# Kernel optimization log

Hardware: AMD Instinct MI355X
Metric: run time of the kernel (lower is better)

The kernel has to match this reference:

```python
import jax, jax.numpy as jnp
import numpy as np
import math

IN_C, OUT_C, K, STYLE_DIM = 512, 512, 3, 512
EPS = 1e-8
SCALE = 1.0 / math.sqrt(IN_C * K * K)


def setup_inputs() -> dict:
    key = jax.random.key(0)
    k1, k2, k3, k4, k5 = jax.random.split(key, 5)
    x = jax.random.normal(k1, (8, IN_C, 64, 64), dtype=jnp.float32)
    style = jax.random.normal(k2, (8, STYLE_DIM), dtype=jnp.float32)
    weight = jax.random.normal(k3, (1, OUT_C, IN_C, K, K), dtype=jnp.float32)
    # nn.Linear(style_dim, in_channels): weight [in_channels, style_dim], bias [in_channels]
    lim = 1.0 / math.sqrt(STYLE_DIM)
    style_w = jax.random.uniform(k4, (IN_C, STYLE_DIM), dtype=jnp.float32, minval=-lim, maxval=lim)
    style_b = jax.random.uniform(k5, (IN_C,), dtype=jnp.float32, minval=-lim, maxval=lim)
    return {"x": x, "style": style, "weight": weight, "style_w": style_w, "style_b": style_b}


def _conv_one(xi, wi):
    # xi: [C,H,W], wi: [O,I,K,K]
    out = jax.lax.conv_general_dilated(
        xi[None], wi, window_strides=(1, 1), padding="SAME",
        dimension_numbers=("NCHW", "OIHW", "NCHW"))
    return out[0]


def reference(x, style, weight, style_w, style_b):
    N = x.shape[0]
    s = style @ style_w.T + style_b                      # [N, C_in]
    w = weight * SCALE                                    # [1,O,I,K,K]
    w = w * s[:, None, :, None, None]                     # [N,O,I,K,K]
    demod = jax.lax.rsqrt(jnp.sum(w * w, axis=(2, 3, 4)) + EPS)  # [N,O]
    w = w * demod[:, :, None, None, None]
    out = jax.vmap(_conv_one)(x, w)                       # [N,O,H,W]
    return out
```

## Files before the change

kernel.cpp:

```cpp
#include <hip/hip_runtime.h>
#include <stdint.h>

typedef unsigned short u16;
typedef __bf16 bf16x8 __attribute__((ext_vector_type(8)));
typedef float f32x4 __attribute__((ext_vector_type(4)));

#define SCALE_F 0.014731391274719742f

#define S_OFF   0u
#define WM_OFF  1081344u
#define XS_OFF  38830080u
#define WS_NEED 74514432u

__device__ __forceinline__ u16 f2bf(float f) {
  union { float f; uint32_t u; } c; c.f = f;
  return (u16)((c.u + 0x7FFFu + ((c.u >> 16) & 1u)) >> 16);
}

__device__ __forceinline__ void gload16(const void* g, void* l) {
  __builtin_amdgcn_global_load_lds(
      (const __attribute__((address_space(1))) uint32_t*)g,
      (__attribute__((address_space(3))) uint32_t*)l, 16, 0, 0);
}

__global__ void k_style(const float* __restrict__ style, const float* __restrict__ sw,
                        const float* __restrict__ sb, float* __restrict__ s) {
  int t = blockIdx.x * 256 + threadIdx.x;
  int n = t >> 9, c = t & 511;
  const float4* wr = (const float4*)(sw + (size_t)c * 512);
  const float4* st = (const float4*)(style + (size_t)n * 512);
  float acc = 0.f;
  #pragma unroll 4
  for (int d = 0; d < 128; ++d) {
    float4 a = st[d], b = wr[d];
    acc += a.x * b.x + a.y * b.y + a.z * b.z + a.w * b.w;
  }
  s[t] = acc + sb[c];
}

__global__ __launch_bounds__(256) void k_wmod3(
    const float* __restrict__ w, const float* __restrict__ s, u16* __restrict__ wm) {
  __shared__ float wlds[4608];
  __shared__ float slds[4096];
  __shared__ float red[8][4];
  __shared__ float dmv_sh[8];
  const uint32_t o = blockIdx.x, t = threadIdx.x;
  const uint32_t lane = t & 63u, wv = t >> 6;
  #pragma unroll
  for (uint32_t c = 0; c < 18u; ++c)
    wlds[c * 256u + t] = w[(size_t)o * 4608u + c * 256u + t] * SCALE_F;
  #pragma unroll
  for (uint32_t c = 0; c < 16u; ++c)
    slds[c * 256u + t] = s[c * 256u + t];
  __syncthreads();
  float part[8] = {0.f, 0.f, 0.f, 0.f, 0.f, 0.f, 0.f, 0.f};
  #pragma unroll
  for (uint32_t hh = 0; hh < 2u; ++hh) {
    uint32_t i = hh * 256u + t;
    float q = 0.f;
    #pragma unroll
    for (uint32_t r = 0; r < 9u; ++r) { float a = wlds[i * 9u + r]; q += a * a; }
    #pragma unroll
    for (uint32_t nn = 0; nn < 8u; ++nn) {
      float sv = slds[nn * 512u + i];
      part[nn] += q * sv * sv;
    }
  }
  #pragma unroll
  for (uint32_t nn = 0; nn < 8u; ++nn) {
    float v = part[nn];
    #pragma unroll
    for (uint32_t off = 32u; off >= 1u; off >>= 1) v += __shfl_down(v, off);
    if (lane == 0u) red[nn][wv] = v;
  }
  __syncthreads();
  if (t < 8u)
    dmv_sh[t] = rsqrtf(red[t][0] + red[t][1] + red[t][2] + red[t][3] + 1e-8f);
  __syncthreads();
  float dmv[8];
  #pragma unroll
  for (uint32_t nn = 0; nn < 8u; ++nn) dmv[nn] = dmv_sh[nn];
  #pragma unroll 2
  for (uint32_t c = 0; c < 18u; ++c) {
    uint32_t idx = c * 256u + t;
    uint32_t i = idx & 511u, r = idx >> 9;
    float wvv = wlds[i * 9u + r];
    #pragma unroll
    for (uint32_t nn = 0; nn < 8u; ++nn)
      wm[((size_t)nn * 512u + o) * 4608u + idx] = f2bf(wvv * slds[nn * 512u + i] * dmv[nn]);
  }
}

__global__ void k_border(u16* __restrict__ xs) {
  uint32_t tg = blockIdx.x * 256u + threadIdx.x;
  uint32_t q = tg >> 6;
  uint32_t r = tg & 63u;
  uint32_t n = q / 260u, b = q % 260u;
  uint32_t h, w;
  if (b < 66u)        { h = 0u;  w = b; }
  else if (b < 132u)  { h = 65u; w = b - 66u; }
  else { uint32_t c = b - 132u; h = 1u + (c >> 1); w = (c & 1u) * 65u; }
  uint4 z = {0u, 0u, 0u, 0u};
  *(uint4*)(xs + (((size_t)n * 66u + h) * 66u + w) * 512u + r * 8u) = z;
}

__global__ __launch_bounds__(256) void k_xpose(const float* __restrict__ x,
                                               u16* __restrict__ xs) {
  __shared__ u16 tile[64][512];
  uint32_t b = blockIdx.x, n = b >> 6, hs = b & 63u;
  uint32_t t = threadIdx.x;
  const float* xr = x + ((size_t)n * 512u * 64u + hs) * 64u;
  uint32_t w4 = (t & 15u) * 4u;
  uint32_t ib = (t >> 4) * 8u;
  #pragma unroll
  for (uint32_t p = 0; p < 4u; ++p) {
    uint32_t i0 = p * 128u + ib;
    float4 v[8];
    #pragma unroll
    for (uint32_t j = 0; j < 8u; ++j)
      v[j] = *(const float4*)(xr + (size_t)(i0 + j) * 4096u + w4);
    #pragma unroll
    for (uint32_t k = 0; k < 4u; ++k) {
      union { u16 h[8]; uint4 q; } pk;
      #pragma unroll
      for (uint32_t j = 0; j < 8u; ++j) {
        float f = (k == 0u) ? v[j].x : (k == 1u) ? v[j].y : (k == 2u) ? v[j].z : v[j].w;
        pk.h[j] = f2bf(f);
      }
      *(uint4*)&tile[w4 + k][i0] = pk.q;
    }
  }
  __syncthreads();
  u16* orow = xs + (((size_t)n * 66u + hs + 1u) * 66u + 1u) * 512u;
  #pragma unroll
  for (uint32_t p = 0; p < 16u; ++p) {
    uint32_t idx = p * 256u + t;
    uint32_t w = idx >> 6, i8 = (idx & 63u) * 8u;
    *(bf16x8*)(orow + (size_t)w * 512u + i8) = *(const bf16x8*)(&tile[w][i8]);
  }
}

__global__ __launch_bounds__(512, 2) void k_conv8(
    const u16* __restrict__ Wm, const u16* __restrict__ Xs, float* __restrict__ out)
{
  extern __shared__ u16 smem[];
  u16* As = smem;
  u16* Bs = smem + 32768;

  const uint32_t bid = blockIdx.x;
  const uint32_t swz = (bid & 7u) * 32u + (bid >> 3);
  const uint32_t n = swz >> 5, ot = (swz >> 4) & 1u, pt = swz & 15u;

  const uint32_t tid = threadIdx.x;
  const uint32_t wid = tid >> 6, lane = tid & 63u;
  const uint32_t l16 = lane & 15u, lg = lane >> 4;
  const uint32_t wm = wid >> 2, wn = wid & 3u;

  const u16* wmn = Wm + (size_t)n * 512u * 4608u;
  const u16* xsn = Xs + (size_t)n * 66u * 66u * 512u;

  f32x4 acc[8][4];
  f32x4 zero = {0.f, 0.f, 0.f, 0.f};
  #pragma unroll
  for (int m = 0; m < 8; ++m)
    #pragma unroll
    for (int nn = 0; nn < 4; ++nn) acc[m][nn] = zero;

  auto stageA = [&](uint32_t Tt, uint32_t half) {
    if (Tt >= 72u) return;
    const uint32_t buf = Tt & 1u;
    const uint32_t r = Tt >> 3, i0 = (Tt & 7u) << 6;
    const uint32_t kh = r / 3u, kw = r % 3u;
    #pragma unroll
    for (uint32_t j = 0; j < 2u; ++j) {
      const uint32_t sl = tid + j * 512u;
      const uint32_t row = sl >> 3, cl = sl & 7u;
      const uint32_t csrc = cl ^ (row & 7u);
      const uint32_t R = half * 128u + row;
      const uint32_t hp = pt * 4u + (R >> 6) + kh, wp = (R & 63u) + kw;
      gload16(xsn + ((size_t)hp * 66u + wp) * 512u + i0 + csrc * 8u,
              As + buf * 16384u + half * 8192u + (wid * 64u + j * 512u) * 8u);
    }
  };
  auto stageB = [&](uint32_t Tt, uint32_t half) {
    if (Tt >= 72u) return;
    const uint32_t buf = Tt & 1u;
    const uint32_t r = Tt >> 3, i0 = (Tt & 7u) << 6;
    #pragma unroll
    for (uint32_t j = 0; j < 2u; ++j) {
      const uint32_t sl = tid + j * 512u;
      const uint32_t row = sl >> 3, cl = sl & 7u;
      const uint32_t csrc = cl ^ (row & 7u);
      const uint32_t o = ot * 256u + half * 128u + row;
      gload16(wmn + (size_t)o * 4608u + r * 512u + i0 + csrc * 8u,
              Bs + buf * 16384u + half * 8192u + (wid * 64u + j * 512u) * 8u);
    }
  };

  stageA(0u, 0u); stageA(0u, 1u); stageB(0u, 0u); stageB(0u, 1u);
  stageA(1u, 0u); stageA(1u, 1u);
  asm volatile("s_waitcnt vmcnt(4)" ::: "memory");
  __builtin_amdgcn_s_barrier();

  bf16x8 a[8][2], b01[2][2], b23[2][2];

  for (uint32_t T = 0; T < 72u; ++T) {
    const uint32_t buf = T & 1u;
    const u16* Ab = As + buf * 16384u;
    const u16* Bb = Bs + buf * 16384u;

    #pragma unroll
    for (uint32_t m = 0; m < 4u; ++m) {
      const uint32_t row = wm * 128u + m * 16u + l16;
      #pragma unroll
      for (uint32_t k = 0; k < 2u; ++k) {
        const uint32_t c = (k * 4u + lg) ^ (row & 7u);
        a[m][k] = *(const bf16x8*)(Ab + row * 64u + c * 8u);
      }
    }
    #pragma unroll
    for (uint32_t nn = 0; nn < 2u; ++nn) {
      const uint32_t row = wn * 64u + nn * 16u + l16;
      #pragma unroll
      for (uint32_t k = 0; k < 2u; ++k) {
        const uint32_t c = (k * 4u + lg) ^ (row & 7u);
        b01[nn][k] = *(const bf16x8*)(Bb + row * 64u + c * 8u);
      }
    }
    stageB(T + 1u, 0u);
    __builtin_amdgcn_s_barrier();
    asm volatile("s_waitcnt lgkmcnt(0)" ::: "memory");
    __builtin_amdgcn_sched_barrier(0);
    __builtin_amdgcn_s_setprio(1);
    #pragma unroll
    for (uint32_t m = 0; m < 4u; ++m)
      #pragma unroll
      for (uint32_t nn = 0; nn < 2u; ++nn)
        #pragma unroll
        for (uint32_t k = 0; k < 2u; ++k)
          acc[m][nn] = __builtin_amdgcn_mfma_f32_16x16x32_bf16(a[m][k], b01[nn][k], acc[m][nn], 0, 0, 0);
    __builtin_amdgcn_s_setprio(0);
    __builtin_amdgcn_s_barrier();

    #pragma unroll
    for (uint32_t m = 0; m < 4u; ++m) {
      const uint32_t row = wm * 128u + (m + 4u) * 16u + l16;
      #pragma unroll
      for (uint32_t k = 0; k < 2u; ++k) {
        const uint32_t c = (k * 4u + lg) ^ (row & 7u);
        a[m + 4u][k] = *(const bf16x8*)(Ab + row * 64u + c * 8u);
      }
    }
    stageB(T + 1u, 1u);
    __builtin_amdgcn_s_barrier();
    asm volatile("s_waitcnt lgkmcnt(0)" ::: "memory");
    __builtin_amdgcn_sched_barrier(0);
    __builtin_amdgcn_s_setprio(1);
    #pragma unroll
    for (uint32_t m = 0; m < 4u; ++m)
      #pragma unroll
      for (uint32_t nn = 0; nn < 2u; ++nn)
        #pragma unroll
        for (uint32_t k = 0; k < 2u; ++k)
          acc[m + 4u][nn] = __builtin_amdgcn_mfma_f32_16x16x32_bf16(a[m + 4u][k], b01[nn][k], acc[m + 4u][nn], 0, 0, 0);
    __builtin_amdgcn_s_setprio(0);
    __builtin_amdgcn_s_barrier();

    #pragma unroll
    for (uint32_t nn = 0; nn < 2u; ++nn) {
      const uint32_t row = wn * 64u + (nn + 2u) * 16u + l16;
      #pragma unroll
      for (uint32_t k = 0; k < 2u; ++k) {
        const uint32_t c = (k * 4u + lg) ^ (row & 7u);
        b23[nn][k] = *(const bf16x8*)(Bb + row * 64u + c * 8u);
      }
    }
    stageA(T + 2u, 0u);
    __builtin_amdgcn_s_barrier();
    asm volatile("s_waitcnt lgkmcnt(0)" ::: "memory");
    __builtin_amdgcn_sched_barrier(0);
    __builtin_amdgcn_s_setprio(1);
    #pragma unroll
    for (uint32_t m = 0; m < 4u; ++m)
      #pragma unroll
      for (uint32_t nn = 0; nn < 2u; ++nn)
        #pragma unroll
        for (uint32_t k = 0; k < 2u; ++k)
          acc[m][nn + 2u] = __builtin_amdgcn_mfma_f32_16x16x32_bf16(a[m][k], b23[nn][k], acc[m][nn + 2u], 0, 0, 0);
    __builtin_amdgcn_s_setprio(0);
    __builtin_amdgcn_s_barrier();

    stageA(T + 2u, 1u);
    __builtin_amdgcn_s_barrier();
    __builtin_amdgcn_s_setprio(1);
    #pragma unroll
    for (uint32_t m = 0; m < 4u; ++m)
      #pragma unroll
      for (uint32_t nn = 0; nn < 2u; ++nn)
        #pragma unroll
        for (uint32_t k = 0; k < 2u; ++k)
          acc[m + 4u][nn + 2u] = __builtin_amdgcn_mfma_f32_16x16x32_bf16(a[m + 4u][k], b23[nn][k], acc[m + 4u][nn + 2u], 0, 0, 0);
    __builtin_amdgcn_s_setprio(0);
    if (T < 70u) {
      asm volatile("s_waitcnt vmcnt(4)" ::: "memory");
    } else {
      asm volatile("s_waitcnt vmcnt(0)" ::: "memory");
    }
    __builtin_amdgcn_s_barrier();
  }

  float* op = out + ((size_t)n * 512u + ot * 256u + wn * 64u) * 4096u + pt * 256u + wm * 128u;
  #pragma unroll
  for (uint32_t m = 0; m < 8u; ++m)
    #pragma unroll
    for (uint32_t nn = 0; nn < 4u; ++nn)
      *(f32x4*)(op + (size_t)(nn * 16u + l16) * 4096u + m * 16u + lg * 4u) = acc[m][nn];
}

extern "C" void kernel_launch(void* const* d_in, const int* in_sizes, int n_in,
                              void* d_out, int out_size, void* d_ws, size_t ws_size,
                              hipStream_t stream) {
  const float* x       = (const float*)d_in[0];
  const float* style   = (const float*)d_in[1];
  const float* weight  = (const float*)d_in[2];
  const float* style_w = (const float*)d_in[3];
  const float* style_b = (const float*)d_in[4];
  float* out = (float*)d_out;

  if (ws_size < (size_t)WS_NEED) return;

  char* ws = (char*)d_ws;
  float* s  = (float*)(ws + S_OFF);
  u16*   wm = (u16*)(ws + WM_OFF);
  u16*   xs = (u16*)(ws + XS_OFF);

  (void)hipFuncSetAttribute((const void*)k_conv8,
                            hipFuncAttributeMaxDynamicSharedMemorySize, 131072);

  hipLaunchKernelGGL(k_style,  dim3(16),   dim3(256), 0, stream, style, style_w, style_b, s);
  hipLaunchKernelGGL(k_wmod3,  dim3(512),  dim3(256), 0, stream, weight, s, wm);
  hipLaunchKernelGGL(k_border, dim3(520),  dim3(256), 0, stream, xs);
  hipLaunchKernelGGL(k_xpose,  dim3(512),  dim3(256), 0, stream, x, xs);
  hipLaunchKernelGGL(k_conv8,  dim3(256),  dim3(512), 131072, stream, wm, xs, out);
}
```

Before: 301.5 us.

## Fold style modulation into input and demod into output epilogue

Instead of building a per-sample modulated weight tensor (8x512x4608 bf16), the style scale is applied to the input activations during the transpose, and the demodulation factor is applied to the conv accumulators at store time. The conv then reads a single shared bf16 weight tensor for all samples, cutting weight-preparation writes and the weight traffic in the GEMM, and shrinking the workspace. Rounding changes slightly because the bf16 quantization now happens on x*s and on the unmodulated weights.

New measurement: 288.6 us. -4.3%, faster.

```diff
diff --git a/kernel.cpp b/kernel.cpp
--- a/kernel.cpp
+++ b/kernel.cpp
@@ -8,9 +8,10 @@
 #define SCALE_F 0.014731391274719742f
 
 #define S_OFF   0u
-#define WM_OFF  1081344u
-#define XS_OFF  38830080u
-#define WS_NEED 74514432u
+#define DM_OFF  16384u
+#define WT_OFF  32768u
+#define XS_OFF  4751360u
+#define WS_NEED 40435712u
 
 __device__ __forceinline__ u16 f2bf(float f) {
   union { float f; uint32_t u; } c; c.f = f;
@@ -38,12 +39,12 @@
   s[t] = acc + sb[c];
 }
 
-__global__ __launch_bounds__(256) void k_wmod3(
-    const float* __restrict__ w, const float* __restrict__ s, u16* __restrict__ wm) {
+__global__ __launch_bounds__(256) void k_wt(
+    const float* __restrict__ w, const float* __restrict__ s,
+    u16* __restrict__ wt, float* __restrict__ dm) {
   __shared__ float wlds[4608];
   __shared__ float slds[4096];
   __shared__ float red[8][4];
-  __shared__ float dmv_sh[8];
   const uint32_t o = blockIdx.x, t = threadIdx.x;
   const uint32_t lane = t & 63u, wv = t >> 6;
   #pragma unroll
@@ -75,19 +76,12 @@
   }
   __syncthreads();
   if (t < 8u)
-    dmv_sh[t] = rsqrtf(red[t][0] + red[t][1] + red[t][2] + red[t][3] + 1e-8f);
-  __syncthreads();
-  float dmv[8];
-  #pragma unroll
-  for (uint32_t nn = 0; nn < 8u; ++nn) dmv[nn] = dmv_sh[nn];
+    dm[t * 512u + o] = rsqrtf(red[t][0] + red[t][1] + red[t][2] + red[t][3] + 1e-8f);
   #pragma unroll 2
   for (uint32_t c = 0; c < 18u; ++c) {
     uint32_t idx = c * 256u + t;
     uint32_t i = idx & 511u, r = idx >> 9;
-    float wvv = wlds[i * 9u + r];
-    #pragma unroll
-    for (uint32_t nn = 0; nn < 8u; ++nn)
-      wm[((size_t)nn * 512u + o) * 4608u + idx] = f2bf(wvv * slds[nn * 512u + i] * dmv[nn]);
+    wt[(size_t)o * 4608u + idx] = f2bf(wlds[i * 9u + r]);
   }
 }
 
@@ -105,6 +99,7 @@
 }
 
 __global__ __launch_bounds__(256) void k_xpose(const float* __restrict__ x,
+                                               const float* __restrict__ s,
                                                u16* __restrict__ xs) {
   __shared__ u16 tile[64][512];
   uint32_t b = blockIdx.x, n = b >> 6, hs = b & 63u;
@@ -112,6 +107,12 @@
   const float* xr = x + ((size_t)n * 512u * 64u + hs) * 64u;
   uint32_t w4 = (t & 15u) * 4u;
   uint32_t ib = (t >> 4) * 8u;
+  float sv[4][8];
+  #pragma unroll
+  for (uint32_t p = 0; p < 4u; ++p)
+    #pragma unroll
+    for (uint32_t j = 0; j < 8u; ++j)
+      sv[p][j] = s[n * 512u + p * 128u + ib + j];
   #pragma unroll
   for (uint32_t p = 0; p < 4u; ++p) {
     uint32_t i0 = p * 128u + ib;
@@ -125,7 +126,7 @@
       #pragma unroll
       for (uint32_t j = 0; j < 8u; ++j) {
         float f = (k == 0u) ? v[j].x : (k == 1u) ? v[j].y : (k == 2u) ? v[j].z : v[j].w;
-        pk.h[j] = f2bf(f);
+        pk.h[j] = f2bf(f * sv[p][j]);
       }
       *(uint4*)&tile[w4 + k][i0] = pk.q;
     }
@@ -141,7 +142,8 @@
 }
 
 __global__ __launch_bounds__(512, 2) void k_conv8(
-    const u16* __restrict__ Wm, const u16* __restrict__ Xs, float* __restrict__ out)
+    const u16* __restrict__ Wt, const u16* __restrict__ Xs,
+    const float* __restrict__ Dm, float* __restrict__ out)
 {
   extern __shared__ u16 smem[];
   u16* As = smem;
@@ -156,7 +158,6 @@
   const uint32_t l16 = lane & 15u, lg = lane >> 4;
   const uint32_t wm = wid >> 2, wn = wid & 3u;
 
-  const u16* wmn = Wm + (size_t)n * 512u * 4608u;
   const u16* xsn = Xs + (size_t)n * 66u * 66u * 512u;
 
   f32x4 acc[8][4];
@@ -192,7 +193,7 @@
       const uint32_t row = sl >> 3, cl = sl & 7u;
       const uint32_t csrc = cl ^ (row & 7u);
       const uint32_t o = ot * 256u + half * 128u + row;
-      gload16(wmn + (size_t)o * 4608u + r * 512u + i0 + csrc * 8u,
+      gload16(Wt + (size_t)o * 4608u + r * 512u + i0 + csrc * 8u,
               Bs + buf * 16384u + half * 8192u + (wid * 64u + j * 512u) * 8u);
     }
   };
@@ -309,12 +310,16 @@
     __builtin_amdgcn_s_barrier();
   }
 
+  float dmv[4];
+  #pragma unroll
+  for (uint32_t nn = 0; nn < 4u; ++nn)
+    dmv[nn] = Dm[n * 512u + ot * 256u + wn * 64u + nn * 16u + l16];
   float* op = out + ((size_t)n * 512u + ot * 256u + wn * 64u) * 4096u + pt * 256u + wm * 128u;
   #pragma unroll
   for (uint32_t m = 0; m < 8u; ++m)
     #pragma unroll
     for (uint32_t nn = 0; nn < 4u; ++nn)
-      *(f32x4*)(op + (size_t)(nn * 16u + l16) * 4096u + m * 16u + lg * 4u) = acc[m][nn];
+      *(f32x4*)(op + (size_t)(nn * 16u + l16) * 4096u + m * 16u + lg * 4u) = acc[m][nn] * dmv[nn];
 }
 
 extern "C" void kernel_launch(void* const* d_in, const int* in_sizes, int n_in,
@@ -331,15 +336,16 @@
 
   char* ws = (char*)d_ws;
   float* s  = (float*)(ws + S_OFF);
-  u16*   wm = (u16*)(ws + WM_OFF);
+  float* dm = (float*)(ws + DM_OFF);
+  u16*   wt = (u16*)(ws + WT_OFF);
   u16*   xs = (u16*)(ws + XS_OFF);
 
   (void)hipFuncSetAttribute((const void*)k_conv8,
                             hipFuncAttributeMaxDynamicSharedMemorySize, 131072);
 
   hipLaunchKernelGGL(k_style,  dim3(16),   dim3(256), 0, stream, style, style_w, style_b, s);
-  hipLaunchKernelGGL(k_wmod3,  dim3(512),  dim3(256), 0, stream, weight, s, wm);
+  hipLaunchKernelGGL(k_wt,     dim3(512),  dim3(256), 0, stream, weight, s, wt, dm);
   hipLaunchKernelGGL(k_border, dim3(520),  dim3(256), 0, stream, xs);
-  hipLaunchKernelGGL(k_xpose,  dim3(512),  dim3(256), 0, stream, x, xs);
-  hipLaunchKernelGGL(k_conv8,  dim3(256),  dim3(512), 131072, stream, wm, xs, out);
-}
+  hipLaunchKernelGGL(k_xpose,  dim3(512),  dim3(256), 0, stream, x, s, xs);
+  hipLaunchKernelGGL(k_conv8,  dim3(256),  dim3(512), 131072, stream, wt, xs, dm, out);
+}
```
